# Performance work log

Hardware: AMD Instinct MI355X
Metric: run time of the kernel (lower is better)

## Reference

```python
import jax, jax.numpy as jnp
import numpy as np

N, E, F, T, H = 100000, 3_200_000, 64, 12, 32


def _lin(k, fin, fout):
    s = 1.0 / np.sqrt(fin)
    k1, k2 = jax.random.split(k)
    W = jax.random.uniform(k1, (fin, fout), jnp.float32, -s, s)
    b = jax.random.uniform(k2, (fout,), jnp.float32, -s, s)
    return W, b


def _lstm_w(k, fin):
    s = 1.0 / np.sqrt(H)
    k1, k2, k3, k4 = jax.random.split(k, 4)
    return (jax.random.uniform(k1, (4 * H, fin), jnp.float32, -s, s),
            jax.random.uniform(k2, (4 * H, H), jnp.float32, -s, s),
            jax.random.uniform(k3, (4 * H,), jnp.float32, -s, s),
            jax.random.uniform(k4, (4 * H,), jnp.float32, -s, s))


def setup_inputs() -> dict:
    key = jax.random.key(0)
    ks = jax.random.split(key, 12)
    x = jax.random.normal(ks[0], (N, F), jnp.float32)
    edge_index = jax.random.randint(ks[1], (2, E), 0, N, dtype=jnp.int32)
    W_fp, b_fp = _lin(ks[2], F, 64)
    W_g1, b_g1 = _lin(ks[3], 64, 64)
    W_g2, b_g2 = _lin(ks[4], 64, 32)
    W_g3, b_g3 = _lin(ks[5], 32, 16)
    W_tp, b_tp = _lin(ks[6], 1, 16)
    Wih0, Whh0, bih0, bhh0 = _lstm_w(ks[7], 16)
    Wih1, Whh1, bih1, bhh1 = _lstm_w(ks[8], H)
    W_fc1, b_fc1 = _lin(ks[9], H, 16)
    W_fc2, b_fc2 = _lin(ks[10], 16, 1)
    return dict(x=x, edge_index=edge_index, W_fp=W_fp, b_fp=b_fp,
                W_g1=W_g1, b_g1=b_g1, W_g2=W_g2, b_g2=b_g2, W_g3=W_g3, b_g3=b_g3,
                W_tp=W_tp, b_tp=b_tp,
                Wih0=Wih0, Whh0=Whh0, bih0=bih0, bhh0=bhh0,
                Wih1=Wih1, Whh1=Whh1, bih1=bih1, bhh1=bhh1,
                W_fc1=W_fc1, b_fc1=b_fc1, W_fc2=W_fc2, b_fc2=b_fc2)


def reference(x, edge_index, W_fp, b_fp, W_g1, b_g1, W_g2, b_g2, W_g3, b_g3,
              W_tp, b_tp, Wih0, Whh0, bih0, bhh0, Wih1, Whh1, bih1, bhh1,
              W_fc1, b_fc1, W_fc2, b_fc2):
    n = x.shape[0]
    loops = jnp.arange(n, dtype=edge_index.dtype)
    src = jnp.concatenate([edge_index[0], loops])  # self-loops, PyG GCNConv default
    dst = jnp.concatenate([edge_index[1], loops])
    deg = jax.ops.segment_sum(jnp.ones_like(src, dtype=x.dtype), dst, num_segments=n)
    dis = deg ** -0.5  # deg >= 1 because of self-loops
    norm = dis[src] * dis[dst]  # [E+N]

    def gcn(h, W, b):
        h = h @ W  # transform then propagate (PyG order)
        agg = jax.ops.segment_sum(h[src] * norm[:, None], dst, num_segments=n)
        return agg + b

    h = jax.nn.relu(x @ W_fp + b_fp)
    h = jax.nn.relu(gcn(h, W_g1, b_g1))        # dropout inactive (eval mode)
    h = jax.nn.relu(gcn(h, W_g2, b_g2))
    h_gcn = jax.nn.relu(gcn(h, W_g3, b_g3))    # NOTE: overwritten in original forward (dead)

    # temporal branch: last T raw features -> [N, T, 1] -> proj to 16
    t = x[:, -T:].reshape(n, T, 1) @ W_tp + b_tp  # [N, T, 16]

    def step(carry, xt):
        h0, c0, h1, c1 = carry
        g = xt @ Wih0.T + h0 @ Whh0.T + (bih0 + bhh0)
        i, f, gg, o = jnp.split(g, 4, axis=-1)  # torch gate order i,f,g,o
        c0 = jax.nn.sigmoid(f) * c0 + jax.nn.sigmoid(i) * jnp.tanh(gg)
        h0 = jax.nn.sigmoid(o) * jnp.tanh(c0)
        g = h0 @ Wih1.T + h1 @ Whh1.T + (bih1 + bhh1)
        i, f, gg, o = jnp.split(g, 4, axis=-1)
        c1 = jax.nn.sigmoid(f) * c1 + jax.nn.sigmoid(i) * jnp.tanh(gg)
        h1 = jax.nn.sigmoid(o) * jnp.tanh(c1)
        return (h0, c0, h1, c1), None

    z = jnp.zeros((n, H), x.dtype)
    (h0, c0, h1, c1), _ = jax.lax.scan(step, (z, z, z, z), jnp.swapaxes(t, 0, 1))
    out = jax.nn.relu(h1 @ W_fc1 + b_fc1) @ W_fc2 + b_fc2  # [N, 1]
    return out
```

## Files before the change

kernel.cpp:

```cpp
#include <hip/hip_runtime.h>


#define TSTEPS 12
#define BS 512
#define NPB (BS / 4)

__device__ __forceinline__ float fsig(float x) {
    float e = __expf(-x);
    return __builtin_amdgcn_rcpf(1.0f + e);
}

__device__ __forceinline__ float ftanh(float x) {
    float ax = fabsf(x);
    float e = __expf(-2.0f * ax);
    float r = (1.0f - e) * __builtin_amdgcn_rcpf(1.0f + e);
    return x < 0.0f ? -r : r;
}

__global__ void precomp_kernel(const float* __restrict__ Wih0,
                               const float* __restrict__ Wtp,
                               const float* __restrict__ btp,
                               const float* __restrict__ bih0,
                               const float* __restrict__ bhh0,
                               const float* __restrict__ bih1,
                               const float* __restrict__ bhh1,
                               float* __restrict__ ws) {
    int r = threadIdx.x;
    if (r < 128) {
        float a = 0.0f, c = 0.0f;
#pragma unroll
        for (int k = 0; k < 16; ++k) {
            float w = Wih0[r * 16 + k];
            a += w * Wtp[k];
            c += w * btp[k];
        }
        const int g4 = r >> 5;
        const int j  = r & 31;
        ws[j * 8 + g4]       = a;
        ws[j * 8 + 4 + g4]   = c + bih0[r] + bhh0[r];
        ws[256 + j * 4 + g4] = bih1[r] + bhh1[r];
    }
}

__device__ __forceinline__ float dot8(const float4 a0, const float4 a1,
                                      const float h[8]) {
    return a0.x*h[0] + a0.y*h[1] + a0.z*h[2] + a0.w*h[3]
         + a1.x*h[4] + a1.y*h[5] + a1.z*h[6] + a1.w*h[7];
}

__device__ __forceinline__ float rs4(float v0, float v1, float v2, float v3,
                                     bool hi2, bool hi1) {
    float sa = hi2 ? v0 : v2;
    float ka = hi2 ? v2 : v0;
    float sb = hi2 ? v1 : v3;
    float kb = hi2 ? v3 : v1;
    float u0 = ka + __shfl_xor(sa, 2);
    float u1 = kb + __shfl_xor(sb, 2);
    float sc = hi1 ? u0 : u1;
    float kc = hi1 ? u1 : u0;
    return kc + __shfl_xor(sc, 1);
}

__device__ __forceinline__ void l0pair(const float* __restrict__ sW,
                                       int jj, int so8, int offA, int offB,
                                       const float h[8], bool hi2, bool hi1,
                                       float& SA, float& SB) {
    float4 a0[4], a1[4], b0[4], b1[4];
#pragma unroll
    for (int g = 0; g < 4; ++g) {
        const float* wa = &sW[(g * 8 + jj + offA) * 32 + so8];
        const float* wb = &sW[(g * 8 + jj + offB) * 32 + so8];
        a0[g] = ((const float4*)wa)[0]; a1[g] = ((const float4*)wa)[1];
        b0[g] = ((const float4*)wb)[0]; b1[g] = ((const float4*)wb)[1];
    }
    float pa[4], pb[4];
#pragma unroll
    for (int g = 0; g < 4; ++g) {
        pa[g] = dot8(a0[g], a1[g], h);
        pb[g] = dot8(b0[g], b1[g], h);
    }
    SA = rs4(pa[0], pa[1], pa[2], pa[3], hi2, hi1);
    SB = rs4(pb[0], pb[1], pb[2], pb[3], hi2, hi1);
}

__device__ __forceinline__ float l1gate(const float* __restrict__ sW,
                                        int jj, int so8, int off,
                                        const float h0[8], const float h1[8],
                                        bool hi2, bool hi1) {
    float4 a0[4], a1[4], b0[4], b1[4];
#pragma unroll
    for (int g = 0; g < 4; ++g) {
        const float* ax = &sW[4096 + (g * 8 + jj + off) * 32 + so8];
        const float* bx = &sW[8192 + (g * 8 + jj + off) * 32 + so8];
        a0[g] = ((const float4*)ax)[0]; a1[g] = ((const float4*)ax)[1];
        b0[g] = ((const float4*)bx)[0]; b1[g] = ((const float4*)bx)[1];
    }
    float p[4];
#pragma unroll
    for (int g = 0; g < 4; ++g)
        p[g] = dot8(a0[g], a1[g], h0) + dot8(b0[g], b1[g], h1);
    return rs4(p[0], p[1], p[2], p[3], hi2, hi1);
}

__global__ __launch_bounds__(BS) void lstm_kernel(
    const float* __restrict__ x,
    const float* __restrict__ Whh0,
    const float* __restrict__ Wih1,
    const float* __restrict__ Whh1,
    const float* __restrict__ Wfc1,
    const float* __restrict__ bfc1,
    const float* __restrict__ Wfc2,
    const float* __restrict__ bfc2,
    const float* __restrict__ pre,
    float* __restrict__ out, int N)
{
    __shared__ __align__(16) float sW[12288];
    __shared__ float sc0[8 * BS];
    __shared__ float sc1[8 * BS];

    const int tid = threadIdx.x;
#pragma unroll
    for (int i = 0; i < 8; ++i) sW[i * BS + tid]        = Whh0[i * BS + tid];
#pragma unroll
    for (int i = 0; i < 8; ++i) sW[4096 + i * BS + tid] = Wih1[i * BS + tid];
#pragma unroll
    for (int i = 0; i < 8; ++i) sW[8192 + i * BS + tid] = Whh1[i * BS + tid];
#pragma unroll
    for (int jj = 0; jj < 8; ++jj) {
        sc0[jj * BS + tid] = 0.0f;
        sc1[jj * BS + tid] = 0.0f;
    }
    __syncthreads();

    const int s    = tid & 3;
    const int node = tid >> 2;
    const int so8  = s * 8;
    const bool hi2 = (s & 2) != 0;
    const bool hi1 = (s & 1) != 0;
    const int n  = blockIdx.x * NPB + node;
    const int nn = (n < N) ? n : (N > 0 ? N - 1 : 0);
    const float* xr = x + (size_t)nn * 64 + 52;

    float h0r[8], h1r[8], hn[8];
#pragma unroll
    for (int k = 0; k < 8; ++k) { h0r[k] = 0.0f; h1r[k] = 0.0f; }

#pragma unroll 1
    for (int t = 0; t < TSTEPS; ++t) {
        const float xval = xr[t];

#pragma unroll
        for (int jj = 0; jj < 8; ++jj) {
            const int jown = so8 + jj;
            float SI, SF, SG, SO;
            l0pair(sW, jj, so8,  0, 32, h0r, hi2, hi1, SI, SF);
            __builtin_amdgcn_sched_barrier(0);
            l0pair(sW, jj, so8, 64, 96, h0r, hi2, hi1, SG, SO);
            __builtin_amdgcn_sched_barrier(0);
            const float4 pA = ((const float4*)pre)[jown * 2];
            const float4 pC = ((const float4*)pre)[jown * 2 + 1];
            const float gi = SI + pC.x + xval * pA.x;
            const float gf = SF + pC.y + xval * pA.y;
            const float gG = SG + pC.z + xval * pA.z;
            const float go = SO + pC.w + xval * pA.w;
            const int ci = jj * BS + tid;
            const float cc = fsig(gf) * sc0[ci] + fsig(gi) * ftanh(gG);
            sc0[ci] = cc;
            hn[jj]  = fsig(go) * ftanh(cc);
        }
#pragma unroll
        for (int k = 0; k < 8; ++k) h0r[k] = hn[k];

#pragma unroll
        for (int jj = 0; jj < 8; ++jj) {
            const int jown = so8 + jj;
            const float SI = l1gate(sW, jj, so8,  0, h0r, h1r, hi2, hi1);
            __builtin_amdgcn_sched_barrier(0);
            const float SF = l1gate(sW, jj, so8, 32, h0r, h1r, hi2, hi1);
            __builtin_amdgcn_sched_barrier(0);
            const float SG = l1gate(sW, jj, so8, 64, h0r, h1r, hi2, hi1);
            __builtin_amdgcn_sched_barrier(0);
            const float SO = l1gate(sW, jj, so8, 96, h0r, h1r, hi2, hi1);
            __builtin_amdgcn_sched_barrier(0);
            const float4 pD = ((const float4*)(pre + 256))[jown];
            const float gi = SI + pD.x;
            const float gf = SF + pD.y;
            const float gG = SG + pD.z;
            const float go = SO + pD.w;
            const int ci = jj * BS + tid;
            const float cc = fsig(gf) * sc1[ci] + fsig(gi) * ftanh(gG);
            sc1[ci] = cc;
            hn[jj]  = fsig(go) * ftanh(cc);
        }
#pragma unroll
        for (int k = 0; k < 8; ++k) h1r[k] = hn[k];
    }

    float am[16];
#pragma unroll
    for (int m = 0; m < 16; ++m) am[m] = 0.0f;
#pragma unroll 1
    for (int kk = 0; kk < 8; ++kk) {
        const float* row = Wfc1 + (size_t)(so8 + kk) * 16;
        const float4 r0 = ((const float4*)row)[0];
        const float4 r1 = ((const float4*)row)[1];
        const float4 r2 = ((const float4*)row)[2];
        const float4 r3 = ((const float4*)row)[3];
        const float hv = h1r[kk];
        am[ 0] += r0.x*hv; am[ 1] += r0.y*hv; am[ 2] += r0.z*hv; am[ 3] += r0.w*hv;
        am[ 4] += r1.x*hv; am[ 5] += r1.y*hv; am[ 6] += r1.z*hv; am[ 7] += r1.w*hv;
        am[ 8] += r2.x*hv; am[ 9] += r2.y*hv; am[10] += r2.z*hv; am[11] += r2.w*hv;
        am[12] += r3.x*hv; am[13] += r3.y*hv; am[14] += r3.z*hv; am[15] += r3.w*hv;
    }
    float acc = bfc2[0];
#pragma unroll
    for (int m = 0; m < 16; ++m) {
        float a = am[m];
        a += __shfl_xor(a, 1); a += __shfl_xor(a, 2);
        acc += fmaxf(a + bfc1[m], 0.0f) * Wfc2[m];
    }
    if (s == 0 && n < N) out[n] = acc;
}

extern "C" void kernel_launch(void* const* d_in, const int* in_sizes, int n_in,
                              void* d_out, int out_size, void* d_ws, size_t ws_size,
                              hipStream_t stream) {
    (void)n_in; (void)out_size; (void)ws_size;
    const float* x    = (const float*)d_in[0];
    const float* Wtp  = (const float*)d_in[10];
    const float* btp  = (const float*)d_in[11];
    const float* Wih0 = (const float*)d_in[12];
    const float* Whh0 = (const float*)d_in[13];
    const float* bih0 = (const float*)d_in[14];
    const float* bhh0 = (const float*)d_in[15];
    const float* Wih1 = (const float*)d_in[16];
    const float* Whh1 = (const float*)d_in[17];
    const float* bih1 = (const float*)d_in[18];
    const float* bhh1 = (const float*)d_in[19];
    const float* Wfc1 = (const float*)d_in[20];
    const float* bfc1 = (const float*)d_in[21];
    const float* Wfc2 = (const float*)d_in[22];
    const float* bfc2 = (const float*)d_in[23];

    float* out = (float*)d_out;
    float* pre = (float*)d_ws;

    const int N = in_sizes[0] / 64;

    precomp_kernel<<<1, 128, 0, stream>>>(Wih0, Wtp, btp, bih0, bhh0, bih1, bhh1, pre);
    lstm_kernel<<<(N + NPB - 1) / NPB, BS, 0, stream>>>(
        x, Whh0, Wih1, Whh1, Wfc1, bfc1, Wfc2, bfc2, pre, out, N);
}
```

Measured before the change: 1.241 ms.

## Process two nodes per thread group to reuse LDS weight loads

Each 4-lane group now handles two nodes (A and B, 64 slots apart). Every weight float4 read from shared memory feeds dot products for both nodes, which halves LDS weight traffic per node. The block shrinks to 256 threads while still covering 128 nodes. In exchange, register pressure roughly doubles for the hidden states, which may lower occupancy.

Result: slower. 1.407 ms (+13.4%).

```diff
diff --git a/kernel.cpp b/kernel.cpp
--- a/kernel.cpp
+++ b/kernel.cpp
@@ -2,8 +2,8 @@
 
 
 #define TSTEPS 12
-#define BS 512
-#define NPB (BS / 4)
+#define BS 256
+#define NPB 128
 
 __device__ __forceinline__ float fsig(float x) {
     float e = __expf(-x);
@@ -59,47 +59,6 @@
     float sc = hi1 ? u0 : u1;
     float kc = hi1 ? u1 : u0;
     return kc + __shfl_xor(sc, 1);
-}
-
-__device__ __forceinline__ void l0pair(const float* __restrict__ sW,
-                                       int jj, int so8, int offA, int offB,
-                                       const float h[8], bool hi2, bool hi1,
-                                       float& SA, float& SB) {
-    float4 a0[4], a1[4], b0[4], b1[4];
-#pragma unroll
-    for (int g = 0; g < 4; ++g) {
-        const float* wa = &sW[(g * 8 + jj + offA) * 32 + so8];
-        const float* wb = &sW[(g * 8 + jj + offB) * 32 + so8];
-        a0[g] = ((const float4*)wa)[0]; a1[g] = ((const float4*)wa)[1];
-        b0[g] = ((const float4*)wb)[0]; b1[g] = ((const float4*)wb)[1];
-    }
-    float pa[4], pb[4];
-#pragma unroll
-    for (int g = 0; g < 4; ++g) {
-        pa[g] = dot8(a0[g], a1[g], h);
-        pb[g] = dot8(b0[g], b1[g], h);
-    }
-    SA = rs4(pa[0], pa[1], pa[2], pa[3], hi2, hi1);
-    SB = rs4(pb[0], pb[1], pb[2], pb[3], hi2, hi1);
-}
-
-__device__ __forceinline__ float l1gate(const float* __restrict__ sW,
-                                        int jj, int so8, int off,
-                                        const float h0[8], const float h1[8],
-                                        bool hi2, bool hi1) {
-    float4 a0[4], a1[4], b0[4], b1[4];
-#pragma unroll
-    for (int g = 0; g < 4; ++g) {
-        const float* ax = &sW[4096 + (g * 8 + jj + off) * 32 + so8];
-        const float* bx = &sW[8192 + (g * 8 + jj + off) * 32 + so8];
-        a0[g] = ((const float4*)ax)[0]; a1[g] = ((const float4*)ax)[1];
-        b0[g] = ((const float4*)bx)[0]; b1[g] = ((const float4*)bx)[1];
-    }
-    float p[4];
-#pragma unroll
-    for (int g = 0; g < 4; ++g)
-        p[g] = dot8(a0[g], a1[g], h0) + dot8(b0[g], b1[g], h1);
-    return rs4(p[0], p[1], p[2], p[3], hi2, hi1);
 }
 
 __global__ __launch_bounds__(BS) void lstm_kernel(
@@ -115,111 +74,211 @@
     float* __restrict__ out, int N)
 {
     __shared__ __align__(16) float sW[12288];
-    __shared__ float sc0[8 * BS];
-    __shared__ float sc1[8 * BS];
+    __shared__ float sc0[16 * BS];
+    __shared__ float sc1[16 * BS];
 
     const int tid = threadIdx.x;
 #pragma unroll
-    for (int i = 0; i < 8; ++i) sW[i * BS + tid]        = Whh0[i * BS + tid];
-#pragma unroll
-    for (int i = 0; i < 8; ++i) sW[4096 + i * BS + tid] = Wih1[i * BS + tid];
-#pragma unroll
-    for (int i = 0; i < 8; ++i) sW[8192 + i * BS + tid] = Whh1[i * BS + tid];
+    for (int i = 0; i < 16; ++i) sW[i * BS + tid]        = Whh0[i * BS + tid];
+#pragma unroll
+    for (int i = 0; i < 16; ++i) sW[4096 + i * BS + tid] = Wih1[i * BS + tid];
+#pragma unroll
+    for (int i = 0; i < 16; ++i) sW[8192 + i * BS + tid] = Whh1[i * BS + tid];
 #pragma unroll
     for (int jj = 0; jj < 8; ++jj) {
-        sc0[jj * BS + tid] = 0.0f;
-        sc1[jj * BS + tid] = 0.0f;
+        sc0[jj * BS + tid] = 0.0f;  sc0[2048 + jj * BS + tid] = 0.0f;
+        sc1[jj * BS + tid] = 0.0f;  sc1[2048 + jj * BS + tid] = 0.0f;
     }
     __syncthreads();
 
     const int s    = tid & 3;
-    const int node = tid >> 2;
+    const int slot = tid >> 2;
     const int so8  = s * 8;
     const bool hi2 = (s & 2) != 0;
     const bool hi1 = (s & 1) != 0;
-    const int n  = blockIdx.x * NPB + node;
-    const int nn = (n < N) ? n : (N > 0 ? N - 1 : 0);
-    const float* xr = x + (size_t)nn * 64 + 52;
-
-    float h0r[8], h1r[8], hn[8];
-#pragma unroll
-    for (int k = 0; k < 8; ++k) { h0r[k] = 0.0f; h1r[k] = 0.0f; }
+    const int nA = blockIdx.x * NPB + slot;
+    const int nB = nA + 64;
+    const int nnA = (nA < N) ? nA : (N > 0 ? N - 1 : 0);
+    const int nnB = (nB < N) ? nB : (N > 0 ? N - 1 : 0);
+    const float* xrA = x + (size_t)nnA * 64 + 52;
+    const float* xrB = x + (size_t)nnB * 64 + 52;
+
+    float h0A[8], h0B[8], h1A[8], h1B[8], hnA[8], hnB[8];
+#pragma unroll
+    for (int k = 0; k < 8; ++k) { h0A[k] = 0.0f; h0B[k] = 0.0f; h1A[k] = 0.0f; h1B[k] = 0.0f; }
 
 #pragma unroll 1
     for (int t = 0; t < TSTEPS; ++t) {
-        const float xval = xr[t];
+        const float xvA = xrA[t];
+        const float xvB = xrB[t];
 
 #pragma unroll
         for (int jj = 0; jj < 8; ++jj) {
             const int jown = so8 + jj;
-            float SI, SF, SG, SO;
-            l0pair(sW, jj, so8,  0, 32, h0r, hi2, hi1, SI, SF);
-            __builtin_amdgcn_sched_barrier(0);
-            l0pair(sW, jj, so8, 64, 96, h0r, hi2, hi1, SG, SO);
-            __builtin_amdgcn_sched_barrier(0);
-            const float4 pA = ((const float4*)pre)[jown * 2];
-            const float4 pC = ((const float4*)pre)[jown * 2 + 1];
-            const float gi = SI + pC.x + xval * pA.x;
-            const float gf = SF + pC.y + xval * pA.y;
-            const float gG = SG + pC.z + xval * pA.z;
-            const float go = SO + pC.w + xval * pA.w;
-            const int ci = jj * BS + tid;
-            const float cc = fsig(gf) * sc0[ci] + fsig(gi) * ftanh(gG);
-            sc0[ci] = cc;
-            hn[jj]  = fsig(go) * ftanh(cc);
-        }
-#pragma unroll
-        for (int k = 0; k < 8; ++k) h0r[k] = hn[k];
+            float SA[4], SB[4];
+#pragma unroll
+            for (int gate = 0; gate < 4; ++gate) {
+                float4 w0[4], w1[4];
+#pragma unroll
+                for (int g = 0; g < 4; ++g) {
+                    const float* w = &sW[(gate * 32 + g * 8 + jj) * 32 + so8];
+                    w0[g] = ((const float4*)w)[0];
+                    w1[g] = ((const float4*)w)[1];
+                }
+                float pA[4], pB[4];
+#pragma unroll
+                for (int g = 0; g < 4; ++g) {
+                    pA[g] = dot8(w0[g], w1[g], h0A);
+                    pB[g] = dot8(w0[g], w1[g], h0B);
+                }
+                SA[gate] = rs4(pA[0], pA[1], pA[2], pA[3], hi2, hi1);
+                SB[gate] = rs4(pB[0], pB[1], pB[2], pB[3], hi2, hi1);
+                __builtin_amdgcn_sched_barrier(0);
+            }
+            const float4 pAq = ((const float4*)pre)[jown * 2];
+            const float4 pCq = ((const float4*)pre)[jown * 2 + 1];
+            {
+                const float gi = SA[0] + pCq.x + xvA * pAq.x;
+                const float gf = SA[1] + pCq.y + xvA * pAq.y;
+                const float gG = SA[2] + pCq.z + xvA * pAq.z;
+                const float go = SA[3] + pCq.w + xvA * pAq.w;
+                const int ci = jj * BS + tid;
+                const float cc = fsig(gf) * sc0[ci] + fsig(gi) * ftanh(gG);
+                sc0[ci] = cc;
+                hnA[jj] = fsig(go) * ftanh(cc);
+            }
+            {
+                const float gi = SB[0] + pCq.x + xvB * pAq.x;
+                const float gf = SB[1] + pCq.y + xvB * pAq.y;
+                const float gG = SB[2] + pCq.z + xvB * pAq.z;
+                const float go = SB[3] + pCq.w + xvB * pAq.w;
+                const int ci = 2048 + jj * BS + tid;
+                const float cc = fsig(gf) * sc0[ci] + fsig(gi) * ftanh(gG);
+                sc0[ci] = cc;
+                hnB[jj] = fsig(go) * ftanh(cc);
+            }
+        }
+#pragma unroll
+        for (int k = 0; k < 8; ++k) { h0A[k] = hnA[k]; h0B[k] = hnB[k]; }
 
 #pragma unroll
         for (int jj = 0; jj < 8; ++jj) {
             const int jown = so8 + jj;
-            const float SI = l1gate(sW, jj, so8,  0, h0r, h1r, hi2, hi1);
-            __builtin_amdgcn_sched_barrier(0);
-            const float SF = l1gate(sW, jj, so8, 32, h0r, h1r, hi2, hi1);
-            __builtin_amdgcn_sched_barrier(0);
-            const float SG = l1gate(sW, jj, so8, 64, h0r, h1r, hi2, hi1);
-            __builtin_amdgcn_sched_barrier(0);
-            const float SO = l1gate(sW, jj, so8, 96, h0r, h1r, hi2, hi1);
-            __builtin_amdgcn_sched_barrier(0);
+            float SA[4], SB[4];
+#pragma unroll
+            for (int gate = 0; gate < 4; ++gate) {
+                float pA[4], pB[4];
+                {
+                    float4 w0[4], w1[4];
+#pragma unroll
+                    for (int g = 0; g < 4; ++g) {
+                        const float* w = &sW[4096 + (gate * 32 + g * 8 + jj) * 32 + so8];
+                        w0[g] = ((const float4*)w)[0];
+                        w1[g] = ((const float4*)w)[1];
+                    }
+#pragma unroll
+                    for (int g = 0; g < 4; ++g) {
+                        pA[g] = dot8(w0[g], w1[g], h0A);
+                        pB[g] = dot8(w0[g], w1[g], h0B);
+                    }
+                }
+                __builtin_amdgcn_sched_barrier(0);
+                {
+                    float4 w0[4], w1[4];
+#pragma unroll
+                    for (int g = 0; g < 4; ++g) {
+                        const float* w = &sW[8192 + (gate * 32 + g * 8 + jj) * 32 + so8];
+                        w0[g] = ((const float4*)w)[0];
+                        w1[g] = ((const float4*)w)[1];
+                    }
+#pragma unroll
+                    for (int g = 0; g < 4; ++g) {
+                        pA[g] += dot8(w0[g], w1[g], h1A);
+                        pB[g] += dot8(w0[g], w1[g], h1B);
+                    }
+                }
+                SA[gate] = rs4(pA[0], pA[1], pA[2], pA[3], hi2, hi1);
+                SB[gate] = rs4(pB[0], pB[1], pB[2], pB[3], hi2, hi1);
+                __builtin_amdgcn_sched_barrier(0);
+            }
             const float4 pD = ((const float4*)(pre + 256))[jown];
-            const float gi = SI + pD.x;
-            const float gf = SF + pD.y;
-            const float gG = SG + pD.z;
-            const float go = SO + pD.w;
-            const int ci = jj * BS + tid;
-            const float cc = fsig(gf) * sc1[ci] + fsig(gi) * ftanh(gG);
-            sc1[ci] = cc;
-            hn[jj]  = fsig(go) * ftanh(cc);
-        }
-#pragma unroll
-        for (int k = 0; k < 8; ++k) h1r[k] = hn[k];
-    }
-
-    float am[16];
-#pragma unroll
-    for (int m = 0; m < 16; ++m) am[m] = 0.0f;
+            {
+                const float gi = SA[0] + pD.x;
+                const float gf = SA[1] + pD.y;
+                const float gG = SA[2] + pD.z;
+                const float go = SA[3] + pD.w;
+                const int ci = jj * BS + tid;
+                const float cc = fsig(gf) * sc1[ci] + fsig(gi) * ftanh(gG);
+                sc1[ci] = cc;
+                hnA[jj] = fsig(go) * ftanh(cc);
+            }
+            {
+                const float gi = SB[0] + pD.x;
+                const float gf = SB[1] + pD.y;
+                const float gG = SB[2] + pD.z;
+                const float go = SB[3] + pD.w;
+                const int ci = 2048 + jj * BS + tid;
+                const float cc = fsig(gf) * sc1[ci] + fsig(gi) * ftanh(gG);
+                sc1[ci] = cc;
+                hnB[jj] = fsig(go) * ftanh(cc);
+            }
+        }
+#pragma unroll
+        for (int k = 0; k < 8; ++k) { h1A[k] = hnA[k]; h1B[k] = hnB[k]; }
+    }
+
+    {
+        float am[16];
+#pragma unroll
+        for (int m = 0; m < 16; ++m) am[m] = 0.0f;
 #pragma unroll 1
-    for (int kk = 0; kk < 8; ++kk) {
-        const float* row = Wfc1 + (size_t)(so8 + kk) * 16;
-        const float4 r0 = ((const float4*)row)[0];
-        const float4 r1 = ((const float4*)row)[1];
-        const float4 r2 = ((const float4*)row)[2];
-        const float4 r3 = ((const float4*)row)[3];
-        const float hv = h1r[kk];
-        am[ 0] += r0.x*hv; am[ 1] += r0.y*hv; am[ 2] += r0.z*hv; am[ 3] += r0.w*hv;
-        am[ 4] += r1.x*hv; am[ 5] += r1.y*hv; am[ 6] += r1.z*hv; am[ 7] += r1.w*hv;
-        am[ 8] += r2.x*hv; am[ 9] += r2.y*hv; am[10] += r2.z*hv; am[11] += r2.w*hv;
-        am[12] += r3.x*hv; am[13] += r3.y*hv; am[14] += r3.z*hv; am[15] += r3.w*hv;
-    }
-    float acc = bfc2[0];
-#pragma unroll
-    for (int m = 0; m < 16; ++m) {
-        float a = am[m];
-        a += __shfl_xor(a, 1); a += __shfl_xor(a, 2);
-        acc += fmaxf(a + bfc1[m], 0.0f) * Wfc2[m];
-    }
-    if (s == 0 && n < N) out[n] = acc;
+        for (int kk = 0; kk < 8; ++kk) {
+            const float* row = Wfc1 + (size_t)(so8 + kk) * 16;
+            const float4 r0 = ((const float4*)row)[0];
+            const float4 r1 = ((const float4*)row)[1];
+            const float4 r2 = ((const float4*)row)[2];
+            const float4 r3 = ((const float4*)row)[3];
+            const float hv = h1A[kk];
+            am[ 0] += r0.x*hv; am[ 1] += r0.y*hv; am[ 2] += r0.z*hv; am[ 3] += r0.w*hv;
+            am[ 4] += r1.x*hv; am[ 5] += r1.y*hv; am[ 6] += r1.z*hv; am[ 7] += r1.w*hv;
+            am[ 8] += r2.x*hv; am[ 9] += r2.y*hv; am[10] += r2.z*hv; am[11] += r2.w*hv;
+            am[12] += r3.x*hv; am[13] += r3.y*hv; am[14] += r3.z*hv; am[15] += r3.w*hv;
+        }
+        float acc = bfc2[0];
+#pragma unroll
+        for (int m = 0; m < 16; ++m) {
+            float a = am[m];
+            a += __shfl_xor(a, 1); a += __shfl_xor(a, 2);
+            acc += fmaxf(a + bfc1[m], 0.0f) * Wfc2[m];
+        }
+        if (s == 0 && nA < N) out[nA] = acc;
+    }
+    {
+        float am[16];
+#pragma unroll
+        for (int m = 0; m < 16; ++m) am[m] = 0.0f;
+#pragma unroll 1
+        for (int kk = 0; kk < 8; ++kk) {
+            const float* row = Wfc1 + (size_t)(so8 + kk) * 16;
+            const float4 r0 = ((const float4*)row)[0];
+            const float4 r1 = ((const float4*)row)[1];
+            const float4 r2 = ((const float4*)row)[2];
+            const float4 r3 = ((const float4*)row)[3];
+            const float hv = h1B[kk];
+            am[ 0] += r0.x*hv; am[ 1] += r0.y*hv; am[ 2] += r0.z*hv; am[ 3] += r0.w*hv;
+            am[ 4] += r1.x*hv; am[ 5] += r1.y*hv; am[ 6] += r1.z*hv; am[ 7] += r1.w*hv;
+            am[ 8] += r2.x*hv; am[ 9] += r2.y*hv; am[10] += r2.z*hv; am[11] += r2.w*hv;
+            am[12] += r3.x*hv; am[13] += r3.y*hv; am[14] += r3.z*hv; am[15] += r3.w*hv;
+        }
+        float acc = bfc2[0];
+#pragma unroll
+        for (int m = 0; m < 16; ++m) {
+            float a = am[m];
+            a += __shfl_xor(a, 1); a += __shfl_xor(a, 2);
+            acc += fmaxf(a + bfc1[m], 0.0f) * Wfc2[m];
+        }
+        if (s == 0 && nB < N) out[nB] = acc;
+    }
 }
 
 extern "C" void kernel_launch(void* const* d_in, const int* in_sizes, int n_in,
```
